# Kernel tuning notes

Measured on AMD Instinct MI355X. Metric: run time of the kernel, lower is better.

## Reference

```python
import jax, jax.numpy as jnp
import numpy as np

XY = 16   # xy_size
Z = 16    # z_size
S = XY * XY * Z   # num_states = 4096
V = 2048  # num_tokens


def _build_structure():
    # Static 3D-grid neighbor structure (replaces the per-state Python loop).
    h = np.arange(S)
    zc, rem = np.divmod(h, XY * XY)
    yc, xc = np.divmod(rem, XY)
    coords = np.stack([xc, yc, zc], 1)                       # [S,3] (x,y,z)
    offs = np.array([[0, 0, 0], [1, 0, 0], [-1, 0, 0], [0, 1, 0],
                     [0, -1, 0], [0, 0, 1], [0, 0, 2]])       # 7 fixed offsets
    nc = coords[:, None, :] + offs[None]                      # [S,7,3]
    valid = ((nc[..., 0] >= 0) & (nc[..., 0] < XY) &
             (nc[..., 1] >= 0) & (nc[..., 1] < XY) &
             (nc[..., 2] >= 0) & (nc[..., 2] < Z))
    dest = nc[..., 0] + XY * (nc[..., 1] + XY * nc[..., 2])   # flat neighbor idx
    # compact valid neighbors to the front, preserving offset order:
    # j-th valid neighbor consumes logit j (matches logits[h, :len(valid)])
    order = np.argsort(~valid, axis=1, kind='stable')
    tgt = np.take_along_axis(dest, order, axis=1)
    vmask = np.take_along_axis(valid, order, axis=1)
    tgt = np.where(vmask, tgt, S)  # invalid slots -> dummy column S
    return jnp.asarray(tgt), jnp.asarray(vmask)

TGT, VMASK = _build_structure()


def transition_log_p(trans_w):
    # masked log-softmax over the first k valid logits of each row
    logits = jnp.where(VMASK, trans_w, -1e30)
    logp = jax.nn.log_softmax(logits, axis=1)
    logp = jnp.where(VMASK, logp, -jnp.inf)
    T = jnp.full((S, S + 1), -jnp.inf, trans_w.dtype)
    T = T.at[jnp.arange(S)[:, None], TGT].set(logp)
    return T[:, :S]  # [S,S], row h = log p(transition targets of h)


def smoothed_emission(emis_w):
    em = jax.nn.log_softmax(emis_w, axis=-1).reshape(Z, XY, XY, V)
    lv, rv = em[:, :, :1], em[:, :, -1:]
    lh, rh = em[:, :1], em[:, -1:]
    c = jnp.zeros((Z, 1, 1, V), em.dtype)  # log(1)=0 pad, as in the original
    c2 = lambda *a: jnp.concatenate(a, axis=2)
    c1 = lambda *a: jnp.concatenate(a, axis=1)
    up = c1(c2(lv, em, rv), c2(c, rh, c), c2(c, rh, c))
    dn = c1(c2(c, lh, c), c2(c, lh, c), c2(lv, em, rv))
    lf = c1(c2(lh, c, c), c2(em, rv, rv), c2(rh, c, c))
    rt = c1(c2(c, c, lh), c2(lv, lv, em), c2(c, c, rh))
    cr = c1(c2(c, lh, c), c2(lv, em, rv), c2(c, rh, c))
    mean = jax.nn.logsumexp(jnp.stack((up, dn, lf, rt, cr)), axis=0) - jnp.log(5.0)
    return mean[:, 1:-1, 1:-1].reshape(S, V)


def _forward(stories, trans_w, emis_w, prior_w):
    priors = jax.nn.log_softmax(prior_w)                      # [S]
    em = smoothed_emission(emis_w)                            # [S,V]
    padded = jnp.concatenate([em, jnp.zeros((S, 1), em.dtype)], axis=1)  # [S,V+1]
    # per-(story, step) emission log-prob: sum over sentence tokens
    all_emis = padded.T[stories].sum(axis=2)                  # [B,L,S]
    all_emis = jnp.transpose(all_emis, (1, 0, 2))             # [L,B,S]
    T = transition_log_p(trans_w)                             # [S,S]
    amax = jnp.max(T, axis=1, keepdims=True)                  # [S,1], finite (self-loop)
    P = jnp.exp(T - amax)                                     # [S,S]
    score0 = all_emis[0] + priors                             # [B,S]

    def step(score, em_t):
        # new[b,a] = em_t[b,a] + logsumexp_h(T[a,h] + score[b,h])  (stable log-matmul)
        smax = jnp.max(score, axis=1, keepdims=True)          # [B,1]
        new = em_t + jnp.log(jnp.exp(score - smax) @ P.T) + smax + amax.T
        return new, new

    _, rest = jax.lax.scan(step, score0, all_emis[1:])
    return jnp.concatenate([score0[None], rest], axis=0)      # [L,B,S]


def setup_inputs() -> dict:
    key = jax.random.key(0)
    k1, k2, k3, k4 = jax.random.split(key, 4)
    B, L, W = 8, 32, 8
    return {
        "stories_tensor": jax.random.randint(k1, (B, L, W), 0, V + 1, dtype=jnp.int32),
        "story_length": L,
        "trans_w": jax.random.normal(k2, (S, 7), jnp.float32),
        "emis_w": jax.random.normal(k3, (S, V), jnp.float32),
        "prior_w": jax.random.normal(k4, (S,), jnp.float32),
    }


def reference(stories_tensor, story_length, trans_w, emis_w, prior_w):
    assert stories_tensor.shape[1] == story_length
    return _forward(stories_tensor, trans_w, emis_w, prior_w)
```

## Files before the change

kernel.cpp:

```cpp
#include <hip/hip_runtime.h>
#include <math.h>

#define XYD 16
#define ZD 16
#define SS 4096
#define VV 2048
#define BB 8
#define LL 32
#define WW 8
#define VC 32
#define SM_STRIDE 257

#define GUARD_L 16
#define GUARD_R 512
#define EBUF_N (GUARD_L + SS + GUARD_R)

#define BAR() asm volatile("s_waitcnt lgkmcnt(0)\n\ts_barrier" ::: "memory")

__device__ __forceinline__ float b2f(unsigned short u) {
    union { unsigned int i; float f; } x; x.i = ((unsigned int)u) << 16; return x.f;
}
__device__ __forceinline__ unsigned short f2b(float f) {
    union { float f; unsigned int i; } x; x.f = f; return (unsigned short)(x.i >> 16);
}

__global__ void k_logZ(const float* __restrict__ emis_w, float* __restrict__ logZ) {
    int wave = threadIdx.x >> 6;
    int lane = threadIdx.x & 63;
    int row  = blockIdx.x * 4 + wave;
    const float* r = emis_w + (size_t)row * VV;
    float vals[32];
    float m = -INFINITY;
#pragma unroll
    for (int k = 0; k < 8; k++) {
        float4 f = ((const float4*)r)[k * 64 + lane];
        vals[k*4+0] = f.x; vals[k*4+1] = f.y; vals[k*4+2] = f.z; vals[k*4+3] = f.w;
    }
#pragma unroll
    for (int k = 0; k < 32; k++) m = fmaxf(m, vals[k]);
#pragma unroll
    for (int o = 32; o; o >>= 1) m = fmaxf(m, __shfl_xor(m, o));
    float sum = 0.f;
#pragma unroll
    for (int k = 0; k < 32; k++) sum += __expf(vals[k] - m);
#pragma unroll
    for (int o = 32; o; o >>= 1) sum += __shfl_xor(sum, o);
    if (lane == 0) logZ[row] = m + __logf(sum);
}

__global__ void k_smooth(const float* __restrict__ emis_w, const float* __restrict__ logZ,
                         float* __restrict__ smT) {
    __shared__ float tileT[VC * SM_STRIDE];
    int z  = blockIdx.x;
    int v0 = blockIdx.y * VC;
    int tid = threadIdx.x;
    int rsub = tid >> 3;
    int c0   = (tid & 7) * 4;

#pragma unroll
    for (int it = 0; it < 8; it++) {
        int r  = it * 32 + rsub;
        int sg = z * 256 + r;
        float lz = logZ[sg];
        float4 w = *(const float4*)(emis_w + (size_t)sg * VV + v0 + c0);
        tileT[(c0+0)*SM_STRIDE + r] = __expf(w.x - lz);
        tileT[(c0+1)*SM_STRIDE + r] = __expf(w.y - lz);
        tileT[(c0+2)*SM_STRIDE + r] = __expf(w.z - lz);
        tileT[(c0+3)*SM_STRIDE + r] = __expf(w.w - lz);
    }
    __syncthreads();

    int x = tid & 15, y = tid >> 4;
    int sxp = (x < 15) ? tid + 1  : tid;
    int sxm = (x > 0)  ? tid - 1  : tid;
    int syp = (y < 15) ? tid + 16 : tid;
    int sym = (y > 0)  ? tid - 16 : tid;
    float* o = smT + (size_t)v0 * SS + z * 256 + tid;
#pragma unroll
    for (int i = 0; i < VC; i++) {
        const float* tb = tileT + i * SM_STRIDE;
        float s = tb[tid] + tb[sxp] + tb[sxm] + tb[syp] + tb[sym];
        o[(size_t)i * SS] = __logf(s * 0.2f);
    }
}

__global__ void k_emis(const int* __restrict__ stories, const float* __restrict__ smT,
                       float* __restrict__ all_emis) {
    int blk = blockIdx.x;
    int t = blk >> 3, b = blk & 7;
    int tid = threadIdx.x;
    int tok[WW];
#pragma unroll
    for (int w = 0; w < WW; w++) tok[w] = stories[(b * LL + t) * WW + w];
#pragma unroll
    for (int i = 0; i < 4; i++) {
        int s = i * 1024 + tid * 4;
        float4 acc = {0.f, 0.f, 0.f, 0.f};
#pragma unroll
        for (int w = 0; w < WW; w++) {
            if (tok[w] < VV) {
                float4 f = *(const float4*)(smT + (size_t)tok[w] * SS + s);
                acc.x += f.x; acc.y += f.y; acc.z += f.z; acc.w += f.w;
            }
        }
        *(float4*)(all_emis + ((size_t)t * BB + b) * SS + s) = acc;
    }
}

__global__ void __launch_bounds__(1024) k_forward(
    const float* __restrict__ trans_w, const float* __restrict__ prior_w,
    const float* __restrict__ all_emis, float* __restrict__ out) {
    __shared__ __align__(16) unsigned short Ebuf[2][EBUF_N];
    __shared__ float red2[2];
    __shared__ float pr[16];
    int b = blockIdx.x;
    int tid = threadIdx.x;
    int lane = tid & 63, wid = tid >> 6;

    if (tid < GUARD_L) { Ebuf[0][tid] = 0; Ebuf[1][tid] = 0; }
    if (tid < GUARD_R) {
        Ebuf[0][GUARD_L + SS + tid] = 0;
        Ebuf[1][GUARD_L + SS + tid] = 0;
    }

    float pw[28], am[4];
    {
        float w7[28];
        const float4* t4 = (const float4*)(trans_w + (size_t)tid * 28);
#pragma unroll
        for (int k = 0; k < 7; k++) ((float4*)w7)[k] = t4[k];
#pragma unroll
        for (int i = 0; i < 4; i++) {
            int j = tid * 4 + i;
            int xx = j & 15, yy = (j >> 4) & 15, zz = j >> 8;
            bool val[7];
            val[0] = true;
            val[1] = (xx < 15); val[2] = (xx > 0);
            val[3] = (yy < 15); val[4] = (yy > 0);
            val[5] = (zz < 15); val[6] = (zz < 14);
            const float* rw = w7 + i * 7;
            float w[7]; int cnt = 0; float m = -INFINITY;
#pragma unroll
            for (int d = 0; d < 7; d++) { if (val[d]) { w[d] = rw[cnt++]; m = fmaxf(m, w[d]); } }
            float se = 0.f;
#pragma unroll
            for (int d = 0; d < 7; d++) if (val[d]) se += __expf(w[d] - m);
#pragma unroll
            for (int d = 0; d < 7; d++) pw[i*7+d] = val[d] ? __expf(w[d] - m) : 0.f;
            am[i] = -__logf(se);
        }
    }

    float4 pv = ((const float4*)prior_w)[tid];
    const float4* emp = (const float4*)(all_emis + (size_t)b * SS) + tid;
    float4 em = *emp;

    float lm = fmaxf(fmaxf(pv.x, pv.y), fmaxf(pv.z, pv.w));
#pragma unroll
    for (int o = 32; o; o >>= 1) lm = fmaxf(lm, __shfl_xor(lm, o));
    if (lane == 0) pr[wid] = lm;
    __syncthreads();
    float gm = pr[0];
#pragma unroll
    for (int w = 1; w < 16; w++) gm = fmaxf(gm, pr[w]);
    __syncthreads();
    float ls = __expf(pv.x - gm) + __expf(pv.y - gm) + __expf(pv.z - gm) + __expf(pv.w - gm);
#pragma unroll
    for (int o = 32; o; o >>= 1) ls += __shfl_xor(ls, o);
    if (lane == 0) pr[wid] = ls;
    __syncthreads();
    float gs = 0.f;
#pragma unroll
    for (int w = 0; w < 16; w++) gs += pr[w];
    float logZp = gm + __logf(gs);

    float v0 = em.x + pv.x - logZp;
    float v1 = em.y + pv.y - logZp;
    float v2 = em.z + pv.z - logZp;
    float v3 = em.w + pv.w - logZp;
    float4 ov_prev = {v0, v1, v2, v3};
    float4* outp = (float4*)(out + (size_t)b * SS) + tid;

    if (tid == 0) red2[0] = v0;
    __syncthreads();
    float g1 = red2[0];
    float XpPrev = g1;
    float Erx = __expf(v0 - XpPrev), Ery = __expf(v1 - XpPrev);
    float Erz = __expf(v2 - XpPrev), Erw = __expf(v3 - XpPrev);
    {
        ushort4 E;
        E.x = f2b(Erx); E.y = f2b(Ery); E.z = f2b(Erz); E.w = f2b(Erw);
        *(ushort4*)(&Ebuf[0][GUARD_L + 4 * tid]) = E;
    }

    emp += (BB * SS) / 4;
    float4 em_next = *emp;

    int cur = 0;
    for (int t = 1; t < LL; t++) {
        BAR();
        *outp = ov_prev;
        outp += (BB * SS) / 4;

        em = em_next;
        if (t < LL - 1) { emp += (BB * SS) / 4; em_next = *emp; }

        float g0 = red2[cur];
        float Xp = 2.f * g0 - g1;

        const unsigned short* Eb = Ebuf[cur] + GUARD_L + 4 * tid;
        ushort4 YpU = *(const ushort4*)(Eb + 16);
        ushort4 YmU = *(const ushort4*)(Eb - 16);
        ushort4 ZpU = *(const ushort4*)(Eb + 256);
        ushort4 ZqU = *(const ushort4*)(Eb + 512);
        float bx  = b2f(Eb[4]);
        float cxw = b2f(Eb[-1]);

        float a0 = Erx*pw[0]  + Ery*pw[1]  + cxw*pw[2]  + b2f(YpU.x)*pw[3]  + b2f(YmU.x)*pw[4]  + b2f(ZpU.x)*pw[5]  + b2f(ZqU.x)*pw[6];
        float a1 = Ery*pw[7]  + Erz*pw[8]  + Erx*pw[9]  + b2f(YpU.y)*pw[10] + b2f(YmU.y)*pw[11] + b2f(ZpU.y)*pw[12] + b2f(ZqU.y)*pw[13];
        float a2 = Erz*pw[14] + Erw*pw[15] + Ery*pw[16] + b2f(YpU.z)*pw[17] + b2f(YmU.z)*pw[18] + b2f(ZpU.z)*pw[19] + b2f(ZqU.z)*pw[20];
        float a3 = Erw*pw[21] + bx*pw[22]  + Erz*pw[23] + b2f(YpU.w)*pw[24] + b2f(YmU.w)*pw[25] + b2f(ZpU.w)*pw[26] + b2f(ZqU.w)*pw[27];

        v0 = em.x + __logf(a0) + XpPrev + am[0];
        v1 = em.y + __logf(a1) + XpPrev + am[1];
        v2 = em.z + __logf(a2) + XpPrev + am[2];
        v3 = em.w + __logf(a3) + XpPrev + am[3];
        ov_prev.x = v0; ov_prev.y = v1; ov_prev.z = v2; ov_prev.w = v3;

        Erx = __expf(v0 - Xp); Ery = __expf(v1 - Xp);
        Erz = __expf(v2 - Xp); Erw = __expf(v3 - Xp);
        {
            ushort4 E;
            E.x = f2b(Erx); E.y = f2b(Ery); E.z = f2b(Erz); E.w = f2b(Erw);
            *(ushort4*)(&Ebuf[cur ^ 1][GUARD_L + 4 * tid]) = E;
        }
        if (tid == 0) red2[cur ^ 1] = v0;

        g1 = g0; XpPrev = Xp; cur ^= 1;
    }
    *outp = ov_prev;
}

extern "C" void kernel_launch(void* const* d_in, const int* in_sizes, int n_in,
                              void* d_out, int out_size, void* d_ws, size_t ws_size,
                              hipStream_t stream) {
    const int*   stories = (const int*)d_in[0];
    const float* trans_w = (const float*)d_in[2];
    const float* emis_w  = (const float*)d_in[3];
    const float* prior_w = (const float*)d_in[4];
    float* out = (float*)d_out;

    char* ws = (char*)d_ws;
    float* smT      = (float*)(ws);
    float* all_emis = (float*)(ws + (size_t)VV * SS * 4);
    float* logZ     = (float*)(ws + (size_t)VV * SS * 4 + (size_t)LL * BB * SS * 4);

    k_logZ<<<SS / 4, 256, 0, stream>>>(emis_w, logZ);
    k_smooth<<<dim3(ZD, VV / VC), 256, 0, stream>>>(emis_w, logZ, smT);
    k_emis<<<LL * BB, 256, 0, stream>>>(stories, smT, all_emis);
    k_forward<<<BB, 1024, 0, stream>>>(trans_w, prior_w, all_emis, out);
}
```

Before: 156.5 us.

## Store smoothed emission table in bf16 and widen forward kernel to 8 states/thread

The smoothed log-emission table is now written as bf16 instead of fp32, which halves both the write traffic in k_smooth (a 32 MB table) and the gather reads in k_emis. Separately, k_forward and k_emis now process 8 states per thread with 512 threads instead of 4 states with 1024, using wider 16-byte LDS accesses and fewer waves per barrier. The cost is lower precision in the emission sums, since each bf16 log value carries an error that accumulates across up to 8 tokens, plus higher register use in the forward loop.

Measured after the change: 160.1 us. 1.02x slower.

```diff
diff --git a/kernel.cpp b/kernel.cpp
--- a/kernel.cpp
+++ b/kernel.cpp
@@ -17,6 +17,8 @@
 
 #define BAR() asm volatile("s_waitcnt lgkmcnt(0)\n\ts_barrier" ::: "memory")
 
+typedef unsigned short us8 __attribute__((ext_vector_type(8)));
+
 __device__ __forceinline__ float b2f(unsigned short u) {
     union { unsigned int i; float f; } x; x.i = ((unsigned int)u) << 16; return x.f;
 }
@@ -49,7 +51,7 @@
 }
 
 __global__ void k_smooth(const float* __restrict__ emis_w, const float* __restrict__ logZ,
-                         float* __restrict__ smT) {
+                         unsigned short* __restrict__ smTb) {
     __shared__ float tileT[VC * SM_STRIDE];
     int z  = blockIdx.x;
     int v0 = blockIdx.y * VC;
@@ -75,69 +77,76 @@
     int sxm = (x > 0)  ? tid - 1  : tid;
     int syp = (y < 15) ? tid + 16 : tid;
     int sym = (y > 0)  ? tid - 16 : tid;
-    float* o = smT + (size_t)v0 * SS + z * 256 + tid;
+    unsigned short* o = smTb + (size_t)v0 * SS + z * 256 + tid;
 #pragma unroll
     for (int i = 0; i < VC; i++) {
         const float* tb = tileT + i * SM_STRIDE;
         float s = tb[tid] + tb[sxp] + tb[sxm] + tb[syp] + tb[sym];
-        o[(size_t)i * SS] = __logf(s * 0.2f);
-    }
-}
-
-__global__ void k_emis(const int* __restrict__ stories, const float* __restrict__ smT,
-                       float* __restrict__ all_emis) {
+        o[(size_t)i * SS] = f2b(__logf(s * 0.2f));
+    }
+}
+
+__global__ void __launch_bounds__(512) k_emis(
+    const int* __restrict__ stories, const unsigned short* __restrict__ smTb,
+    float* __restrict__ all_emis) {
     int blk = blockIdx.x;
     int t = blk >> 3, b = blk & 7;
     int tid = threadIdx.x;
     int tok[WW];
 #pragma unroll
     for (int w = 0; w < WW; w++) tok[w] = stories[(b * LL + t) * WW + w];
-#pragma unroll
-    for (int i = 0; i < 4; i++) {
-        int s = i * 1024 + tid * 4;
-        float4 acc = {0.f, 0.f, 0.f, 0.f};
-#pragma unroll
-        for (int w = 0; w < WW; w++) {
-            if (tok[w] < VV) {
-                float4 f = *(const float4*)(smT + (size_t)tok[w] * SS + s);
-                acc.x += f.x; acc.y += f.y; acc.z += f.z; acc.w += f.w;
-            }
-        }
-        *(float4*)(all_emis + ((size_t)t * BB + b) * SS + s) = acc;
-    }
-}
-
-__global__ void __launch_bounds__(1024) k_forward(
+    int s0 = tid * 8;
+    float acc[8] = {0.f,0.f,0.f,0.f,0.f,0.f,0.f,0.f};
+#pragma unroll
+    for (int w = 0; w < WW; w++) {
+        if (tok[w] < VV) {
+            us8 u = *(const us8*)(smTb + (size_t)tok[w] * SS + s0);
+#pragma unroll
+            for (int i = 0; i < 8; i++) acc[i] += b2f(u[i]);
+        }
+    }
+    float* dst = all_emis + ((size_t)t * BB + b) * SS + s0;
+    float4 lo = {acc[0], acc[1], acc[2], acc[3]};
+    float4 hi = {acc[4], acc[5], acc[6], acc[7]};
+    ((float4*)dst)[0] = lo;
+    ((float4*)dst)[1] = hi;
+}
+
+__global__ void __launch_bounds__(512) k_forward(
     const float* __restrict__ trans_w, const float* __restrict__ prior_w,
     const float* __restrict__ all_emis, float* __restrict__ out) {
     __shared__ __align__(16) unsigned short Ebuf[2][EBUF_N];
     __shared__ float red2[2];
-    __shared__ float pr[16];
+    __shared__ float pr[8];
     int b = blockIdx.x;
     int tid = threadIdx.x;
     int lane = tid & 63, wid = tid >> 6;
 
     if (tid < GUARD_L) { Ebuf[0][tid] = 0; Ebuf[1][tid] = 0; }
-    if (tid < GUARD_R) {
+    {
         Ebuf[0][GUARD_L + SS + tid] = 0;
         Ebuf[1][GUARD_L + SS + tid] = 0;
     }
 
-    float pw[28], am[4];
-    {
-        float w7[28];
-        const float4* t4 = (const float4*)(trans_w + (size_t)tid * 28);
-#pragma unroll
-        for (int k = 0; k < 7; k++) ((float4*)w7)[k] = t4[k];
-#pragma unroll
-        for (int i = 0; i < 4; i++) {
-            int j = tid * 4 + i;
-            int xx = j & 15, yy = (j >> 4) & 15, zz = j >> 8;
+    float pw[56], am[8];
+    {
+        float w7[56];
+        const float4* t4 = (const float4*)(trans_w + (size_t)tid * 56);
+#pragma unroll
+        for (int k = 0; k < 14; k++) ((float4*)w7)[k] = t4[k];
+        int j0 = tid * 8;
+        int x0 = j0 & 15;
+        int yy = (j0 >> 4) & 15, zz = j0 >> 8;
+        bool vy_p = (yy < 15), vy_m = (yy > 0);
+        bool vz_p = (zz < 15), vz_q = (zz < 14);
+#pragma unroll
+        for (int i = 0; i < 8; i++) {
+            int x = x0 + i;
             bool val[7];
             val[0] = true;
-            val[1] = (xx < 15); val[2] = (xx > 0);
-            val[3] = (yy < 15); val[4] = (yy > 0);
-            val[5] = (zz < 15); val[6] = (zz < 14);
+            val[1] = (x < 15); val[2] = (x > 0);
+            val[3] = vy_p; val[4] = vy_m;
+            val[5] = vz_p; val[6] = vz_q;
             const float* rw = w7 + i * 7;
             float w[7]; int cnt = 0; float m = -INFINITY;
 #pragma unroll
@@ -151,94 +160,117 @@
         }
     }
 
-    float4 pv = ((const float4*)prior_w)[tid];
-    const float4* emp = (const float4*)(all_emis + (size_t)b * SS) + tid;
-    float4 em = *emp;
-
-    float lm = fmaxf(fmaxf(pv.x, pv.y), fmaxf(pv.z, pv.w));
+    float pv[8];
+    {
+        const float4* p4 = (const float4*)prior_w + 2 * tid;
+        ((float4*)pv)[0] = p4[0]; ((float4*)pv)[1] = p4[1];
+    }
+    const float4* emp = (const float4*)(all_emis + (size_t)b * SS) + 2 * tid;
+    float em[8];
+    ((float4*)em)[0] = emp[0]; ((float4*)em)[1] = emp[1];
+
+    float lm = -INFINITY;
+#pragma unroll
+    for (int i = 0; i < 8; i++) lm = fmaxf(lm, pv[i]);
 #pragma unroll
     for (int o = 32; o; o >>= 1) lm = fmaxf(lm, __shfl_xor(lm, o));
     if (lane == 0) pr[wid] = lm;
     __syncthreads();
     float gm = pr[0];
 #pragma unroll
-    for (int w = 1; w < 16; w++) gm = fmaxf(gm, pr[w]);
-    __syncthreads();
-    float ls = __expf(pv.x - gm) + __expf(pv.y - gm) + __expf(pv.z - gm) + __expf(pv.w - gm);
+    for (int w = 1; w < 8; w++) gm = fmaxf(gm, pr[w]);
+    __syncthreads();
+    float ls = 0.f;
+#pragma unroll
+    for (int i = 0; i < 8; i++) ls += __expf(pv[i] - gm);
 #pragma unroll
     for (int o = 32; o; o >>= 1) ls += __shfl_xor(ls, o);
     if (lane == 0) pr[wid] = ls;
     __syncthreads();
     float gs = 0.f;
 #pragma unroll
-    for (int w = 0; w < 16; w++) gs += pr[w];
+    for (int w = 0; w < 8; w++) gs += pr[w];
     float logZp = gm + __logf(gs);
 
-    float v0 = em.x + pv.x - logZp;
-    float v1 = em.y + pv.y - logZp;
-    float v2 = em.z + pv.z - logZp;
-    float v3 = em.w + pv.w - logZp;
-    float4 ov_prev = {v0, v1, v2, v3};
-    float4* outp = (float4*)(out + (size_t)b * SS) + tid;
-
-    if (tid == 0) red2[0] = v0;
+    float v[8], E[8], ov_prev[8];
+#pragma unroll
+    for (int i = 0; i < 8; i++) { v[i] = em[i] + pv[i] - logZp; ov_prev[i] = v[i]; }
+    float4* outp = (float4*)(out + (size_t)b * SS) + 2 * tid;
+
+    if (tid == 0) red2[0] = v[0];
     __syncthreads();
     float g1 = red2[0];
     float XpPrev = g1;
-    float Erx = __expf(v0 - XpPrev), Ery = __expf(v1 - XpPrev);
-    float Erz = __expf(v2 - XpPrev), Erw = __expf(v3 - XpPrev);
-    {
-        ushort4 E;
-        E.x = f2b(Erx); E.y = f2b(Ery); E.z = f2b(Erz); E.w = f2b(Erw);
-        *(ushort4*)(&Ebuf[0][GUARD_L + 4 * tid]) = E;
+#pragma unroll
+    for (int i = 0; i < 8; i++) E[i] = __expf(v[i] - XpPrev);
+    {
+        us8 u;
+#pragma unroll
+        for (int i = 0; i < 8; i++) u[i] = f2b(E[i]);
+        *(us8*)(&Ebuf[0][GUARD_L + 8 * tid]) = u;
     }
 
     emp += (BB * SS) / 4;
-    float4 em_next = *emp;
+    float em_next[8];
+    ((float4*)em_next)[0] = emp[0]; ((float4*)em_next)[1] = emp[1];
 
     int cur = 0;
     for (int t = 1; t < LL; t++) {
         BAR();
-        *outp = ov_prev;
+        outp[0] = ((float4*)ov_prev)[0];
+        outp[1] = ((float4*)ov_prev)[1];
         outp += (BB * SS) / 4;
 
-        em = em_next;
-        if (t < LL - 1) { emp += (BB * SS) / 4; em_next = *emp; }
+#pragma unroll
+        for (int i = 0; i < 8; i++) em[i] = em_next[i];
+        if (t < LL - 1) {
+            emp += (BB * SS) / 4;
+            ((float4*)em_next)[0] = emp[0]; ((float4*)em_next)[1] = emp[1];
+        }
 
         float g0 = red2[cur];
         float Xp = 2.f * g0 - g1;
 
-        const unsigned short* Eb = Ebuf[cur] + GUARD_L + 4 * tid;
-        ushort4 YpU = *(const ushort4*)(Eb + 16);
-        ushort4 YmU = *(const ushort4*)(Eb - 16);
-        ushort4 ZpU = *(const ushort4*)(Eb + 256);
-        ushort4 ZqU = *(const ushort4*)(Eb + 512);
-        float bx  = b2f(Eb[4]);
+        const unsigned short* Eb = Ebuf[cur] + GUARD_L + 8 * tid;
+        us8 YpU = *(const us8*)(Eb + 16);
+        us8 YmU = *(const us8*)(Eb - 16);
+        us8 ZpU = *(const us8*)(Eb + 256);
+        us8 ZqU = *(const us8*)(Eb + 512);
+        float bx  = b2f(Eb[8]);
         float cxw = b2f(Eb[-1]);
 
-        float a0 = Erx*pw[0]  + Ery*pw[1]  + cxw*pw[2]  + b2f(YpU.x)*pw[3]  + b2f(YmU.x)*pw[4]  + b2f(ZpU.x)*pw[5]  + b2f(ZqU.x)*pw[6];
-        float a1 = Ery*pw[7]  + Erz*pw[8]  + Erx*pw[9]  + b2f(YpU.y)*pw[10] + b2f(YmU.y)*pw[11] + b2f(ZpU.y)*pw[12] + b2f(ZqU.y)*pw[13];
-        float a2 = Erz*pw[14] + Erw*pw[15] + Ery*pw[16] + b2f(YpU.z)*pw[17] + b2f(YmU.z)*pw[18] + b2f(ZpU.z)*pw[19] + b2f(ZqU.z)*pw[20];
-        float a3 = Erw*pw[21] + bx*pw[22]  + Erz*pw[23] + b2f(YpU.w)*pw[24] + b2f(YmU.w)*pw[25] + b2f(ZpU.w)*pw[26] + b2f(ZqU.w)*pw[27];
-
-        v0 = em.x + __logf(a0) + XpPrev + am[0];
-        v1 = em.y + __logf(a1) + XpPrev + am[1];
-        v2 = em.z + __logf(a2) + XpPrev + am[2];
-        v3 = em.w + __logf(a3) + XpPrev + am[3];
-        ov_prev.x = v0; ov_prev.y = v1; ov_prev.z = v2; ov_prev.w = v3;
-
-        Erx = __expf(v0 - Xp); Ery = __expf(v1 - Xp);
-        Erz = __expf(v2 - Xp); Erw = __expf(v3 - Xp);
+        float a[8];
+#pragma unroll
+        for (int i = 0; i < 8; i++) {
+            float exp_ = (i < 7) ? E[i + 1] : bx;
+            float exm_ = (i > 0) ? E[i - 1] : cxw;
+            a[i] = E[i]       * pw[i*7+0]
+                 + exp_       * pw[i*7+1]
+                 + exm_       * pw[i*7+2]
+                 + b2f(YpU[i])* pw[i*7+3]
+                 + b2f(YmU[i])* pw[i*7+4]
+                 + b2f(ZpU[i])* pw[i*7+5]
+                 + b2f(ZqU[i])* pw[i*7+6];
+        }
+#pragma unroll
+        for (int i = 0; i < 8; i++) {
+            v[i] = em[i] + __logf(a[i]) + XpPrev + am[i];
+            ov_prev[i] = v[i];
+        }
+#pragma unroll
+        for (int i = 0; i < 8; i++) E[i] = __expf(v[i] - Xp);
         {
-            ushort4 E;
-            E.x = f2b(Erx); E.y = f2b(Ery); E.z = f2b(Erz); E.w = f2b(Erw);
-            *(ushort4*)(&Ebuf[cur ^ 1][GUARD_L + 4 * tid]) = E;
-        }
-        if (tid == 0) red2[cur ^ 1] = v0;
+            us8 u;
+#pragma unroll
+            for (int i = 0; i < 8; i++) u[i] = f2b(E[i]);
+            *(us8*)(&Ebuf[cur ^ 1][GUARD_L + 8 * tid]) = u;
+        }
+        if (tid == 0) red2[cur ^ 1] = v[0];
 
         g1 = g0; XpPrev = Xp; cur ^= 1;
     }
-    *outp = ov_prev;
+    outp[0] = ((float4*)ov_prev)[0];
+    outp[1] = ((float4*)ov_prev)[1];
 }
 
 extern "C" void kernel_launch(void* const* d_in, const int* in_sizes, int n_in,
@@ -251,12 +283,12 @@
     float* out = (float*)d_out;
 
     char* ws = (char*)d_ws;
-    float* smT      = (float*)(ws);
-    float* all_emis = (float*)(ws + (size_t)VV * SS * 4);
-    float* logZ     = (float*)(ws + (size_t)VV * SS * 4 + (size_t)LL * BB * SS * 4);
+    unsigned short* smTb = (unsigned short*)(ws);
+    float* all_emis = (float*)(ws + (size_t)VV * SS * 2);
+    float* logZ     = (float*)(ws + (size_t)VV * SS * 2 + (size_t)LL * BB * SS * 4);
 
     k_logZ<<<SS / 4, 256, 0, stream>>>(emis_w, logZ);
-    k_smooth<<<dim3(ZD, VV / VC), 256, 0, stream>>>(emis_w, logZ, smT);
-    k_emis<<<LL * BB, 256, 0, stream>>>(stories, smT, all_emis);
-    k_forward<<<BB, 1024, 0, stream>>>(trans_w, prior_w, all_emis, out);
-}
+    k_smooth<<<dim3(ZD, VV / VC), 256, 0, stream>>>(emis_w, logZ, smTb);
+    k_emis<<<LL * BB, 512, 0, stream>>>(stories, smTb, all_emis);
+    k_forward<<<BB, 512, 0, stream>>>(trans_w, prior_w, all_emis, out);
+}
```

## Store smoothed emissions as bf16 and move the forward recurrence to linear space

Applied to the files above, without the earlier changes.

The smoothed emission table written by k_smooth is stored as bf16 instead of fp32, halving that 32 MB write and the gather reads in k_emis, which now uses 512 threads with 8-wide loads. The forward kernel keeps its shared-memory buffer in fp32 and carries the next exponentiated state directly as a*exp(em+am+dX), so the per-step expf of the new score is no longer on the chain feeding the barrier. The log outputs are computed off that path. This trades precision in the emission table for bandwidth, and a linear-space recurrence can underflow or overflow if the shift estimate drifts.

New measurement: 152.2 us. -2.7%, faster.

```diff
diff --git a/kernel.cpp b/kernel.cpp
--- a/kernel.cpp
+++ b/kernel.cpp
@@ -17,6 +17,8 @@
 
 #define BAR() asm volatile("s_waitcnt lgkmcnt(0)\n\ts_barrier" ::: "memory")
 
+typedef unsigned short us8 __attribute__((ext_vector_type(8)));
+
 __device__ __forceinline__ float b2f(unsigned short u) {
     union { unsigned int i; float f; } x; x.i = ((unsigned int)u) << 16; return x.f;
 }
@@ -49,7 +51,7 @@
 }
 
 __global__ void k_smooth(const float* __restrict__ emis_w, const float* __restrict__ logZ,
-                         float* __restrict__ smT) {
+                         unsigned short* __restrict__ smTb) {
     __shared__ float tileT[VC * SM_STRIDE];
     int z  = blockIdx.x;
     int v0 = blockIdx.y * VC;
@@ -75,52 +77,55 @@
     int sxm = (x > 0)  ? tid - 1  : tid;
     int syp = (y < 15) ? tid + 16 : tid;
     int sym = (y > 0)  ? tid - 16 : tid;
-    float* o = smT + (size_t)v0 * SS + z * 256 + tid;
+    unsigned short* o = smTb + (size_t)v0 * SS + z * 256 + tid;
 #pragma unroll
     for (int i = 0; i < VC; i++) {
         const float* tb = tileT + i * SM_STRIDE;
         float s = tb[tid] + tb[sxp] + tb[sxm] + tb[syp] + tb[sym];
-        o[(size_t)i * SS] = __logf(s * 0.2f);
-    }
-}
-
-__global__ void k_emis(const int* __restrict__ stories, const float* __restrict__ smT,
-                       float* __restrict__ all_emis) {
+        o[(size_t)i * SS] = f2b(__logf(s * 0.2f));
+    }
+}
+
+__global__ void __launch_bounds__(512) k_emis(
+    const int* __restrict__ stories, const unsigned short* __restrict__ smTb,
+    float* __restrict__ all_emis) {
     int blk = blockIdx.x;
     int t = blk >> 3, b = blk & 7;
     int tid = threadIdx.x;
     int tok[WW];
 #pragma unroll
     for (int w = 0; w < WW; w++) tok[w] = stories[(b * LL + t) * WW + w];
-#pragma unroll
-    for (int i = 0; i < 4; i++) {
-        int s = i * 1024 + tid * 4;
-        float4 acc = {0.f, 0.f, 0.f, 0.f};
-#pragma unroll
-        for (int w = 0; w < WW; w++) {
-            if (tok[w] < VV) {
-                float4 f = *(const float4*)(smT + (size_t)tok[w] * SS + s);
-                acc.x += f.x; acc.y += f.y; acc.z += f.z; acc.w += f.w;
-            }
+    int s0 = tid * 8;
+    float acc[8] = {0.f,0.f,0.f,0.f,0.f,0.f,0.f,0.f};
+#pragma unroll
+    for (int w = 0; w < WW; w++) {
+        if (tok[w] < VV) {
+            us8 u = *(const us8*)(smTb + (size_t)tok[w] * SS + s0);
+#pragma unroll
+            for (int i = 0; i < 8; i++) acc[i] += b2f(u[i]);
         }
-        *(float4*)(all_emis + ((size_t)t * BB + b) * SS + s) = acc;
-    }
+    }
+    float* dst = all_emis + ((size_t)t * BB + b) * SS + s0;
+    float4 lo = {acc[0], acc[1], acc[2], acc[3]};
+    float4 hi = {acc[4], acc[5], acc[6], acc[7]};
+    ((float4*)dst)[0] = lo;
+    ((float4*)dst)[1] = hi;
 }
 
 __global__ void __launch_bounds__(1024) k_forward(
     const float* __restrict__ trans_w, const float* __restrict__ prior_w,
     const float* __restrict__ all_emis, float* __restrict__ out) {
-    __shared__ __align__(16) unsigned short Ebuf[2][EBUF_N];
+    __shared__ __align__(16) float Ebuf[2][EBUF_N];
     __shared__ float red2[2];
     __shared__ float pr[16];
     int b = blockIdx.x;
     int tid = threadIdx.x;
     int lane = tid & 63, wid = tid >> 6;
 
-    if (tid < GUARD_L) { Ebuf[0][tid] = 0; Ebuf[1][tid] = 0; }
+    if (tid < GUARD_L) { Ebuf[0][tid] = 0.f; Ebuf[1][tid] = 0.f; }
     if (tid < GUARD_R) {
-        Ebuf[0][GUARD_L + SS + tid] = 0;
-        Ebuf[1][GUARD_L + SS + tid] = 0;
+        Ebuf[0][GUARD_L + SS + tid] = 0.f;
+        Ebuf[1][GUARD_L + SS + tid] = 0.f;
     }
 
     float pw[28], am[4];
@@ -185,12 +190,11 @@
     __syncthreads();
     float g1 = red2[0];
     float XpPrev = g1;
-    float Erx = __expf(v0 - XpPrev), Ery = __expf(v1 - XpPrev);
-    float Erz = __expf(v2 - XpPrev), Erw = __expf(v3 - XpPrev);
+    float E0 = __expf(v0 - XpPrev), E1 = __expf(v1 - XpPrev);
+    float E2 = __expf(v2 - XpPrev), E3 = __expf(v3 - XpPrev);
     {
-        ushort4 E;
-        E.x = f2b(Erx); E.y = f2b(Ery); E.z = f2b(Erz); E.w = f2b(Erw);
-        *(ushort4*)(&Ebuf[0][GUARD_L + 4 * tid]) = E;
+        float4 E4 = {E0, E1, E2, E3};
+        ((float4*)(Ebuf[0] + GUARD_L))[tid] = E4;
     }
 
     emp += (BB * SS) / 4;
@@ -199,42 +203,45 @@
     int cur = 0;
     for (int t = 1; t < LL; t++) {
         BAR();
+        em = em_next;
+        if (t < LL - 1) { emp += (BB * SS) / 4; em_next = *emp; }
+
+        float g0 = red2[cur];
+        float Xp = 2.f * g0 - g1;
+        float dX = XpPrev - Xp;
+        float F0 = __expf(em.x + am[0] + dX);
+        float F1 = __expf(em.y + am[1] + dX);
+        float F2 = __expf(em.z + am[2] + dX);
+        float F3 = __expf(em.w + am[3] + dX);
+
         *outp = ov_prev;
         outp += (BB * SS) / 4;
 
-        em = em_next;
-        if (t < LL - 1) { emp += (BB * SS) / 4; em_next = *emp; }
-
-        float g0 = red2[cur];
-        float Xp = 2.f * g0 - g1;
-
-        const unsigned short* Eb = Ebuf[cur] + GUARD_L + 4 * tid;
-        ushort4 YpU = *(const ushort4*)(Eb + 16);
-        ushort4 YmU = *(const ushort4*)(Eb - 16);
-        ushort4 ZpU = *(const ushort4*)(Eb + 256);
-        ushort4 ZqU = *(const ushort4*)(Eb + 512);
-        float bx  = b2f(Eb[4]);
-        float cxw = b2f(Eb[-1]);
-
-        float a0 = Erx*pw[0]  + Ery*pw[1]  + cxw*pw[2]  + b2f(YpU.x)*pw[3]  + b2f(YmU.x)*pw[4]  + b2f(ZpU.x)*pw[5]  + b2f(ZqU.x)*pw[6];
-        float a1 = Ery*pw[7]  + Erz*pw[8]  + Erx*pw[9]  + b2f(YpU.y)*pw[10] + b2f(YmU.y)*pw[11] + b2f(ZpU.y)*pw[12] + b2f(ZqU.y)*pw[13];
-        float a2 = Erz*pw[14] + Erw*pw[15] + Ery*pw[16] + b2f(YpU.z)*pw[17] + b2f(YmU.z)*pw[18] + b2f(ZpU.z)*pw[19] + b2f(ZqU.z)*pw[20];
-        float a3 = Erw*pw[21] + bx*pw[22]  + Erz*pw[23] + b2f(YpU.w)*pw[24] + b2f(YmU.w)*pw[25] + b2f(ZpU.w)*pw[26] + b2f(ZqU.w)*pw[27];
-
-        v0 = em.x + __logf(a0) + XpPrev + am[0];
-        v1 = em.y + __logf(a1) + XpPrev + am[1];
-        v2 = em.z + __logf(a2) + XpPrev + am[2];
-        v3 = em.w + __logf(a3) + XpPrev + am[3];
-        ov_prev.x = v0; ov_prev.y = v1; ov_prev.z = v2; ov_prev.w = v3;
-
-        Erx = __expf(v0 - Xp); Ery = __expf(v1 - Xp);
-        Erz = __expf(v2 - Xp); Erw = __expf(v3 - Xp);
+        const float*  Es = Ebuf[cur] + GUARD_L;
+        const float4* Ep = (const float4*)Es;
+        float  bx  = Es[4 * tid + 4];
+        float  cxw = Es[4 * tid - 1];
+        float4 Yp = Ep[tid + 4];
+        float4 Ym = Ep[tid - 4];
+        float4 Zp = Ep[tid + 64];
+        float4 Zq = Ep[tid + 128];
+
+        float a0 = E0*pw[0]  + E1*pw[1]  + cxw*pw[2] + Yp.x*pw[3]  + Ym.x*pw[4]  + Zp.x*pw[5]  + Zq.x*pw[6];
+        float a1 = E1*pw[7]  + E2*pw[8]  + E0*pw[9]  + Yp.y*pw[10] + Ym.y*pw[11] + Zp.y*pw[12] + Zq.y*pw[13];
+        float a2 = E2*pw[14] + E3*pw[15] + E1*pw[16] + Yp.z*pw[17] + Ym.z*pw[18] + Zp.z*pw[19] + Zq.z*pw[20];
+        float a3 = E3*pw[21] + bx*pw[22] + E2*pw[23] + Yp.w*pw[24] + Ym.w*pw[25] + Zp.w*pw[26] + Zq.w*pw[27];
+
+        E0 = a0 * F0; E1 = a1 * F1; E2 = a2 * F2; E3 = a3 * F3;
         {
-            ushort4 E;
-            E.x = f2b(Erx); E.y = f2b(Ery); E.z = f2b(Erz); E.w = f2b(Erw);
-            *(ushort4*)(&Ebuf[cur ^ 1][GUARD_L + 4 * tid]) = E;
+            float4 E4 = {E0, E1, E2, E3};
+            ((float4*)(Ebuf[cur ^ 1] + GUARD_L))[tid] = E4;
         }
-        if (tid == 0) red2[cur ^ 1] = v0;
+        if (tid == 0) red2[cur ^ 1] = em.x + __logf(a0) + XpPrev + am[0];
+
+        ov_prev.x = em.x + __logf(a0) + XpPrev + am[0];
+        ov_prev.y = em.y + __logf(a1) + XpPrev + am[1];
+        ov_prev.z = em.z + __logf(a2) + XpPrev + am[2];
+        ov_prev.w = em.w + __logf(a3) + XpPrev + am[3];
 
         g1 = g0; XpPrev = Xp; cur ^= 1;
     }
@@ -251,12 +258,12 @@
     float* out = (float*)d_out;
 
     char* ws = (char*)d_ws;
-    float* smT      = (float*)(ws);
-    float* all_emis = (float*)(ws + (size_t)VV * SS * 4);
-    float* logZ     = (float*)(ws + (size_t)VV * SS * 4 + (size_t)LL * BB * SS * 4);
+    unsigned short* smTb = (unsigned short*)(ws);
+    float* all_emis = (float*)(ws + (size_t)VV * SS * 2);
+    float* logZ     = (float*)(ws + (size_t)VV * SS * 2 + (size_t)LL * BB * SS * 4);
 
     k_logZ<<<SS / 4, 256, 0, stream>>>(emis_w, logZ);
-    k_smooth<<<dim3(ZD, VV / VC), 256, 0, stream>>>(emis_w, logZ, smT);
-    k_emis<<<LL * BB, 256, 0, stream>>>(stories, smT, all_emis);
+    k_smooth<<<dim3(ZD, VV / VC), 256, 0, stream>>>(emis_w, logZ, smTb);
+    k_emis<<<LL * BB, 512, 0, stream>>>(stories, smTb, all_emis);
     k_forward<<<BB, 1024, 0, stream>>>(trans_w, prior_w, all_emis, out);
 }
```

## Fuse emission gather into forward kernel, store smoothed table as bf16

Applied to the files above, without the earlier changes.

The smoothed emission table is now written as bf16, which halves its write traffic, and the separate k_emis kernel is removed. The forward kernel gathers token rows directly from the table and prefetches the next step's tokens while the current step runs. The recurrence is also reformulated so that the next step's exp values come from a0*exp(em+am+dX), taking the log/exp pair off the critical dependency chain. The costs are bf16 precision loss on the emission log-probs and eight scattered gathers per step inside the serial loop.

Result: slower. 183.7 us (+17.4%).

```diff
diff --git a/kernel.cpp b/kernel.cpp
--- a/kernel.cpp
+++ b/kernel.cpp
@@ -49,7 +49,7 @@
 }
 
 __global__ void k_smooth(const float* __restrict__ emis_w, const float* __restrict__ logZ,
-                         float* __restrict__ smT) {
+                         unsigned short* __restrict__ smTb) {
     __shared__ float tileT[VC * SM_STRIDE];
     int z  = blockIdx.x;
     int v0 = blockIdx.y * VC;
@@ -75,44 +75,23 @@
     int sxm = (x > 0)  ? tid - 1  : tid;
     int syp = (y < 15) ? tid + 16 : tid;
     int sym = (y > 0)  ? tid - 16 : tid;
-    float* o = smT + (size_t)v0 * SS + z * 256 + tid;
+    unsigned short* o = smTb + (size_t)v0 * SS + z * 256 + tid;
 #pragma unroll
     for (int i = 0; i < VC; i++) {
         const float* tb = tileT + i * SM_STRIDE;
         float s = tb[tid] + tb[sxp] + tb[sxm] + tb[syp] + tb[sym];
-        o[(size_t)i * SS] = __logf(s * 0.2f);
-    }
-}
-
-__global__ void k_emis(const int* __restrict__ stories, const float* __restrict__ smT,
-                       float* __restrict__ all_emis) {
-    int blk = blockIdx.x;
-    int t = blk >> 3, b = blk & 7;
-    int tid = threadIdx.x;
-    int tok[WW];
-#pragma unroll
-    for (int w = 0; w < WW; w++) tok[w] = stories[(b * LL + t) * WW + w];
-#pragma unroll
-    for (int i = 0; i < 4; i++) {
-        int s = i * 1024 + tid * 4;
-        float4 acc = {0.f, 0.f, 0.f, 0.f};
-#pragma unroll
-        for (int w = 0; w < WW; w++) {
-            if (tok[w] < VV) {
-                float4 f = *(const float4*)(smT + (size_t)tok[w] * SS + s);
-                acc.x += f.x; acc.y += f.y; acc.z += f.z; acc.w += f.w;
-            }
-        }
-        *(float4*)(all_emis + ((size_t)t * BB + b) * SS + s) = acc;
+        o[(size_t)i * SS] = f2b(__logf(s * 0.2f));
     }
 }
 
 __global__ void __launch_bounds__(1024) k_forward(
     const float* __restrict__ trans_w, const float* __restrict__ prior_w,
-    const float* __restrict__ all_emis, float* __restrict__ out) {
+    const unsigned short* __restrict__ smTb, const int* __restrict__ stories,
+    float* __restrict__ out) {
     __shared__ __align__(16) unsigned short Ebuf[2][EBUF_N];
     __shared__ float red2[2];
     __shared__ float pr[16];
+    __shared__ int toksL[LL * WW];
     int b = blockIdx.x;
     int tid = threadIdx.x;
     int lane = tid & 63, wid = tid >> 6;
@@ -122,6 +101,7 @@
         Ebuf[0][GUARD_L + SS + tid] = 0;
         Ebuf[1][GUARD_L + SS + tid] = 0;
     }
+    if (tid < LL * WW) toksL[tid] = stories[b * LL * WW + tid];
 
     float pw[28], am[4];
     {
@@ -152,8 +132,18 @@
     }
 
     float4 pv = ((const float4*)prior_w)[tid];
-    const float4* emp = (const float4*)(all_emis + (size_t)b * SS) + tid;
-    float4 em = *emp;
+    __syncthreads();
+
+    const unsigned short* smBase = smTb + 4 * tid;
+    float4 em = {0.f, 0.f, 0.f, 0.f};
+#pragma unroll
+    for (int w = 0; w < WW; w++) {
+        int tk = toksL[w];
+        if (tk < VV) {
+            ushort4 u = *(const ushort4*)(smBase + (size_t)tk * SS);
+            em.x += b2f(u.x); em.y += b2f(u.y); em.z += b2f(u.z); em.w += b2f(u.w);
+        }
+    }
 
     float lm = fmaxf(fmaxf(pv.x, pv.y), fmaxf(pv.z, pv.w));
 #pragma unroll
@@ -185,28 +175,50 @@
     __syncthreads();
     float g1 = red2[0];
     float XpPrev = g1;
-    float Erx = __expf(v0 - XpPrev), Ery = __expf(v1 - XpPrev);
-    float Erz = __expf(v2 - XpPrev), Erw = __expf(v3 - XpPrev);
+    float E0 = __expf(v0 - XpPrev), E1 = __expf(v1 - XpPrev);
+    float E2 = __expf(v2 - XpPrev), E3 = __expf(v3 - XpPrev);
     {
         ushort4 E;
-        E.x = f2b(Erx); E.y = f2b(Ery); E.z = f2b(Erz); E.w = f2b(Erw);
+        E.x = f2b(E0); E.y = f2b(E1); E.z = f2b(E2); E.w = f2b(E3);
         *(ushort4*)(&Ebuf[0][GUARD_L + 4 * tid]) = E;
     }
 
-    emp += (BB * SS) / 4;
-    float4 em_next = *emp;
+    ushort4 pf[WW];
+#pragma unroll
+    for (int w = 0; w < WW; w++) {
+        int tk = toksL[WW + w];
+        pf[w] = (tk < VV) ? *(const ushort4*)(smBase + (size_t)tk * SS)
+                          : (ushort4){0, 0, 0, 0};
+    }
 
     int cur = 0;
     for (int t = 1; t < LL; t++) {
         BAR();
+        em.x = 0.f; em.y = 0.f; em.z = 0.f; em.w = 0.f;
+#pragma unroll
+        for (int w = 0; w < WW; w++) {
+            em.x += b2f(pf[w].x); em.y += b2f(pf[w].y);
+            em.z += b2f(pf[w].z); em.w += b2f(pf[w].w);
+        }
+        if (t < LL - 1) {
+#pragma unroll
+            for (int w = 0; w < WW; w++) {
+                int tk = toksL[(t + 1) * WW + w];
+                pf[w] = (tk < VV) ? *(const ushort4*)(smBase + (size_t)tk * SS)
+                                  : (ushort4){0, 0, 0, 0};
+            }
+        }
+
+        float g0 = red2[cur];
+        float Xp = 2.f * g0 - g1;
+        float dX = XpPrev - Xp;
+        float F0 = __expf(em.x + am[0] + dX);
+        float F1 = __expf(em.y + am[1] + dX);
+        float F2 = __expf(em.z + am[2] + dX);
+        float F3 = __expf(em.w + am[3] + dX);
+
         *outp = ov_prev;
         outp += (BB * SS) / 4;
-
-        em = em_next;
-        if (t < LL - 1) { emp += (BB * SS) / 4; em_next = *emp; }
-
-        float g0 = red2[cur];
-        float Xp = 2.f * g0 - g1;
 
         const unsigned short* Eb = Ebuf[cur] + GUARD_L + 4 * tid;
         ushort4 YpU = *(const ushort4*)(Eb + 16);
@@ -216,25 +228,24 @@
         float bx  = b2f(Eb[4]);
         float cxw = b2f(Eb[-1]);
 
-        float a0 = Erx*pw[0]  + Ery*pw[1]  + cxw*pw[2]  + b2f(YpU.x)*pw[3]  + b2f(YmU.x)*pw[4]  + b2f(ZpU.x)*pw[5]  + b2f(ZqU.x)*pw[6];
-        float a1 = Ery*pw[7]  + Erz*pw[8]  + Erx*pw[9]  + b2f(YpU.y)*pw[10] + b2f(YmU.y)*pw[11] + b2f(ZpU.y)*pw[12] + b2f(ZqU.y)*pw[13];
-        float a2 = Erz*pw[14] + Erw*pw[15] + Ery*pw[16] + b2f(YpU.z)*pw[17] + b2f(YmU.z)*pw[18] + b2f(ZpU.z)*pw[19] + b2f(ZqU.z)*pw[20];
-        float a3 = Erw*pw[21] + bx*pw[22]  + Erz*pw[23] + b2f(YpU.w)*pw[24] + b2f(YmU.w)*pw[25] + b2f(ZpU.w)*pw[26] + b2f(ZqU.w)*pw[27];
-
-        v0 = em.x + __logf(a0) + XpPrev + am[0];
-        v1 = em.y + __logf(a1) + XpPrev + am[1];
-        v2 = em.z + __logf(a2) + XpPrev + am[2];
-        v3 = em.w + __logf(a3) + XpPrev + am[3];
-        ov_prev.x = v0; ov_prev.y = v1; ov_prev.z = v2; ov_prev.w = v3;
-
-        Erx = __expf(v0 - Xp); Ery = __expf(v1 - Xp);
-        Erz = __expf(v2 - Xp); Erw = __expf(v3 - Xp);
+        float a0 = E0*pw[0]  + E1*pw[1]  + cxw*pw[2] + b2f(YpU.x)*pw[3]  + b2f(YmU.x)*pw[4]  + b2f(ZpU.x)*pw[5]  + b2f(ZqU.x)*pw[6];
+        float a1 = E1*pw[7]  + E2*pw[8]  + E0*pw[9]  + b2f(YpU.y)*pw[10] + b2f(YmU.y)*pw[11] + b2f(ZpU.y)*pw[12] + b2f(ZqU.y)*pw[13];
+        float a2 = E2*pw[14] + E3*pw[15] + E1*pw[16] + b2f(YpU.z)*pw[17] + b2f(YmU.z)*pw[18] + b2f(ZpU.z)*pw[19] + b2f(ZqU.z)*pw[20];
+        float a3 = E3*pw[21] + bx*pw[22] + E2*pw[23] + b2f(YpU.w)*pw[24] + b2f(YmU.w)*pw[25] + b2f(ZpU.w)*pw[26] + b2f(ZqU.w)*pw[27];
+
+        E0 = a0 * F0; E1 = a1 * F1; E2 = a2 * F2; E3 = a3 * F3;
         {
             ushort4 E;
-            E.x = f2b(Erx); E.y = f2b(Ery); E.z = f2b(Erz); E.w = f2b(Erw);
+            E.x = f2b(E0); E.y = f2b(E1); E.z = f2b(E2); E.w = f2b(E3);
             *(ushort4*)(&Ebuf[cur ^ 1][GUARD_L + 4 * tid]) = E;
         }
-        if (tid == 0) red2[cur ^ 1] = v0;
+        float lg0 = __logf(a0);
+        if (tid == 0) red2[cur ^ 1] = em.x + lg0 + XpPrev + am[0];
+
+        ov_prev.x = em.x + lg0        + XpPrev + am[0];
+        ov_prev.y = em.y + __logf(a1) + XpPrev + am[1];
+        ov_prev.z = em.z + __logf(a2) + XpPrev + am[2];
+        ov_prev.w = em.w + __logf(a3) + XpPrev + am[3];
 
         g1 = g0; XpPrev = Xp; cur ^= 1;
     }
@@ -251,12 +262,10 @@
     float* out = (float*)d_out;
 
     char* ws = (char*)d_ws;
-    float* smT      = (float*)(ws);
-    float* all_emis = (float*)(ws + (size_t)VV * SS * 4);
-    float* logZ     = (float*)(ws + (size_t)VV * SS * 4 + (size_t)LL * BB * SS * 4);
+    unsigned short* smTb = (unsigned short*)(ws);
+    float* logZ = (float*)(ws + (size_t)VV * SS * 2);
 
     k_logZ<<<SS / 4, 256, 0, stream>>>(emis_w, logZ);
-    k_smooth<<<dim3(ZD, VV / VC), 256, 0, stream>>>(emis_w, logZ, smT);
-    k_emis<<<LL * BB, 256, 0, stream>>>(stories, smT, all_emis);
-    k_forward<<<BB, 1024, 0, stream>>>(trans_w, prior_w, all_emis, out);
-}
+    k_smooth<<<dim3(ZD, VV / VC), 256, 0, stream>>>(emis_w, logZ, smTb);
+    k_forward<<<BB, 1024, 0, stream>>>(trans_w, prior_w, smTb, stories, out);
+}
```
